# Kernel tuning notes

Measured on AMD Instinct MI355X. Metric: run time of the kernel, lower is better.

Reference implementation:

```python
import jax, jax.numpy as jnp
import numpy as np

N, L, D = 4, 4096, 1024
H = 16
HD = D // H          # 64
MLP = 4 * D          # 4096
EPS = 1e-5

def log_g(x):
    # torch: where(x>=0, log(relu(x)+0.5), -softplus(-x))
    return jnp.where(x >= 0.0, jnp.log(jax.nn.relu(x) + 0.5), -jax.nn.softplus(-x))

def parallel_scan_log(log_coeffs, log_values):
    # log_coeffs: (B, L, C); log_values: (B, L+1, C)
    a_star = jnp.pad(jnp.cumsum(log_coeffs, axis=1), ((0, 0), (1, 0), (0, 0)))
    log_h = jax.lax.cumlogsumexp(log_values - a_star, axis=1)
    return jnp.exp(a_star[:, 1:] + log_h[:, 1:])

def layer_norm(x, gamma, beta):
    mu = jnp.mean(x, axis=-1, keepdims=True)
    var = jnp.var(x, axis=-1, keepdims=True)
    return (x - mu) * jax.lax.rsqrt(var + EPS) * gamma + beta

def setup_inputs() -> dict:
    key = jax.random.key(0)
    ks = jax.random.split(key, 12)
    s = 0.02
    return {
        "x": jax.random.normal(ks[0], (N, L, D), jnp.float32),
        "h_0": jax.random.normal(ks[1], (N, 1, D), jnp.float32),
        "w_in": jax.random.normal(ks[2], (D, D), jnp.float32) * s,
        "b_in": jnp.zeros((D,), jnp.float32),
        "wz": jax.random.normal(ks[3], (HD, HD), jnp.float32) * s,
        "bz": jnp.zeros((HD,), jnp.float32),
        "wh": jax.random.normal(ks[4], (HD, HD), jnp.float32) * s,
        "bh": jnp.zeros((HD,), jnp.float32),
        "w_out": jax.random.normal(ks[5], (D, D), jnp.float32) * s,
        "b_out": jnp.zeros((D,), jnp.float32),
        "ln1_g": jnp.ones((D,), jnp.float32),
        "ln1_b": jnp.zeros((D,), jnp.float32),
        "ln2_g": jnp.ones((D,), jnp.float32),
        "ln2_b": jnp.zeros((D,), jnp.float32),
        "mw1": jax.random.normal(ks[6], (D, MLP), jnp.float32) * s,
        "mb1": jnp.zeros((MLP,), jnp.float32),
        "mw2": jax.random.normal(ks[7], (MLP, MLP), jnp.float32) * s,
        "mb2": jnp.zeros((MLP,), jnp.float32),
        "mw3": jax.random.normal(ks[8], (MLP, D), jnp.float32) * s,
        "mb3": jnp.zeros((D,), jnp.float32),
    }

def reference(x, h_0, w_in, b_in, wz, bz, wh, bh, w_out, b_out,
              ln1_g, ln1_b, ln2_g, ln2_b, mw1, mb1, mw2, mb2, mw3, mb3):
    n, l, d = x.shape
    rnn_input = layer_norm(x, ln1_g, ln1_b)
    pi = rnn_input @ w_in + b_in                                 # (N,L,D)
    pi = pi.reshape(n, l, H, HD).transpose(0, 2, 1, 3).reshape(n * H, l, HD)
    h0 = h_0.reshape(n, 1, H, HD).transpose(0, 2, 1, 3).reshape(n * H, 1, HD)
    # minGRU in log-space
    k = pi @ wz + bz
    log_z = -jax.nn.softplus(-k)
    log_coeffs = -jax.nn.softplus(k)
    log_h0 = log_g(h0)
    log_th = log_g(pi @ wh + bh)
    h = parallel_scan_log(log_coeffs, jnp.concatenate([log_h0, log_z + log_th], axis=1))
    rnn_states = h.reshape(n, H, l, HD).transpose(0, 2, 1, 3).reshape(n, l, d)
    x = x + (rnn_states @ w_out + b_out)
    mlp_in = layer_norm(x, ln2_g, ln2_b)
    y = jax.nn.silu(mlp_in @ mw1 + mb1)
    y = jax.nn.silu(y @ mw2 + mb2)
    y = y @ mw3 + mb3
    return (x + y, rnn_states)
```

## Files before the change

kernel.cpp:

```cpp
#include <hip/hip_runtime.h>
#include <hip/hip_bf16.h>

typedef __attribute__((ext_vector_type(8))) short short8;
typedef __attribute__((ext_vector_type(4))) float f32x4;
using bf16 = __hip_bfloat16;

#define DEV static __device__ __forceinline__

DEV float bf2f(bf16 v) { return __bfloat162float(v); }
DEV bf16 f2bf(float v) { return __float2bfloat16(v); }

DEV void gld_lds16(const void* g, void* l) {
  __builtin_amdgcn_global_load_lds(
      (const __attribute__((address_space(1))) void*)g,
      (__attribute__((address_space(3))) void*)l, 16, 0, 0);
}

__global__ __launch_bounds__(256)
void wconv_kernel(const float* __restrict__ w, bf16* __restrict__ wT, int K, int N) {
  __shared__ float tile[32][33];
  const int kt = blockIdx.x * 32, nt = blockIdx.y * 32;
  const int tx = threadIdx.x & 31, ty = threadIdx.x >> 5;
#pragma unroll
  for (int i = 0; i < 32; i += 8)
    tile[ty + i][tx] = w[(size_t)(kt + ty + i) * N + nt + tx];
  __syncthreads();
#pragma unroll
  for (int i = 0; i < 32; i += 8)
    wT[(size_t)(nt + ty + i) * K + kt + tx] = f2bf(tile[tx][ty + i]);
}

__global__ __launch_bounds__(256)
void ln_kernel(const float* __restrict__ x, const float* __restrict__ g,
               const float* __restrict__ b, bf16* __restrict__ out) {
  const int row = blockIdx.x;
  const int t = threadIdx.x;
  const float4 v = ((const float4*)(x + (size_t)row * 1024))[t];
  float s = v.x + v.y + v.z + v.w;
  float ss = v.x * v.x + v.y * v.y + v.z * v.z + v.w * v.w;
#pragma unroll
  for (int off = 32; off > 0; off >>= 1) {
    s += __shfl_down(s, off);
    ss += __shfl_down(ss, off);
  }
  __shared__ float red[8];
  if ((t & 63) == 0) { red[(t >> 6) * 2] = s; red[(t >> 6) * 2 + 1] = ss; }
  __syncthreads();
  s = red[0] + red[2] + red[4] + red[6];
  ss = red[1] + red[3] + red[5] + red[7];
  const float mu = s * (1.f / 1024.f);
  const float rstd = rsqrtf(ss * (1.f / 1024.f) - mu * mu + 1e-5f);
  const float4 g4 = ((const float4*)g)[t];
  const float4 b4 = ((const float4*)b)[t];
  struct alignas(8) B4 { bf16 v[4]; } o;
  o.v[0] = f2bf((v.x - mu) * rstd * g4.x + b4.x);
  o.v[1] = f2bf((v.y - mu) * rstd * g4.y + b4.y);
  o.v[2] = f2bf((v.z - mu) * rstd * g4.z + b4.z);
  o.v[3] = f2bf((v.w - mu) * rstd * g4.w + b4.w);
  *(B4*)(out + (size_t)row * 1024 + t * 4) = o;
}

template <int EPI>
__global__ __launch_bounds__(256, 2)
void gemm128(const bf16* __restrict__ A, const bf16* __restrict__ BT,
             const float* __restrict__ bias, const float* __restrict__ res,
             void* __restrict__ C, int M, int N, int K) {
  __shared__ short As[128 * 64];
  __shared__ short Bs[128 * 64];
  const int tid = threadIdx.x;
  const int l = tid & 63;
  const int w = tid >> 6;
  const int wr = w >> 1, wc = w & 1;

  const int nbn = N >> 7;
  const int nwg = gridDim.x;
  const int bid = blockIdx.x;
  const int q = nwg >> 3, r = nwg & 7;
  const int xcd = bid & 7, lin = bid >> 3;
  const int wg = (xcd < r ? xcd * (q + 1) : r * (q + 1) + (xcd - r) * q) + lin;
  const int bm = wg / nbn, bn = wg % nbn;

  const bf16* Ab = A + (size_t)bm * 128 * K;
  const bf16* Bb = BT + (size_t)bn * 128 * K;

  f32x4 acc[4][4];
#pragma unroll
  for (int i = 0; i < 4; ++i)
#pragma unroll
    for (int j = 0; j < 4; ++j) acc[i][j] = (f32x4){0.f, 0.f, 0.f, 0.f};

  const int srow = l >> 3;
  const int scol = (((l & 7) ^ (l >> 3)) << 3);

  for (int k0 = 0; k0 < K; k0 += 64) {
    __syncthreads();
#pragma unroll
    for (int p = 0; p < 4; ++p) {
      const int rowA = p * 32 + w * 8 + srow;
      gld_lds16(Ab + (size_t)rowA * K + k0 + scol, As + (p * 32 + w * 8) * 64);
      gld_lds16(Bb + (size_t)rowA * K + k0 + scol, Bs + (p * 32 + w * 8) * 64);
    }
    __syncthreads();
    const int xr = (l & 7) << 3;
#pragma unroll
    for (int kk = 0; kk < 2; ++kk) {
      short8 fa[4], fb[4];
#pragma unroll
      for (int m = 0; m < 4; ++m)
        fa[m] = *(const short8*)&As[(wr * 64 + m * 16 + (l & 15)) * 64 +
                                    ((kk * 32 + (l >> 4) * 8) ^ xr)];
#pragma unroll
      for (int n = 0; n < 4; ++n)
        fb[n] = *(const short8*)&Bs[(wc * 64 + n * 16 + (l & 15)) * 64 +
                                    ((kk * 32 + (l >> 4) * 8) ^ xr)];
#pragma unroll
      for (int m = 0; m < 4; ++m)
#pragma unroll
        for (int n = 0; n < 4; ++n)
          acc[m][n] = __builtin_amdgcn_mfma_f32_16x16x32_bf16(fa[m], fb[n], acc[m][n], 0, 0, 0);
    }
  }

  const int lc = l & 15;
  const int lr = (l >> 4) * 4;
#pragma unroll
  for (int n = 0; n < 4; ++n) {
    const int col = bn * 128 + wc * 64 + n * 16 + lc;
    const float bv = bias[col];
#pragma unroll
    for (int m = 0; m < 4; ++m) {
      const int row = bm * 128 + wr * 64 + m * 16 + lr;
#pragma unroll
      for (int r2 = 0; r2 < 4; ++r2) {
        float v = acc[m][n][r2] + bv;
        const size_t off = (size_t)(row + r2) * N + col;
        if constexpr (EPI == 1) v = v / (1.f + __expf(-v));
        if constexpr (EPI == 2) {
          ((float*)C)[off] = res[off] + v;
        } else {
          ((bf16*)C)[off] = f2bf(v);
        }
      }
    }
  }
  (void)M;
}

template <int EPI>
__global__ __launch_bounds__(512, 2)
void gemm256(const bf16* __restrict__ A, const bf16* __restrict__ BT,
             const float* __restrict__ bias, const float* __restrict__ res,
             void* __restrict__ C, int M, int N, int K) {
  __shared__ alignas(16) short As[2][256 * 64];
  __shared__ alignas(16) short Bs[2][256 * 64];
  const int tid = threadIdx.x;
  const int l = tid & 63;
  const int w = tid >> 6;
  const int wr = w >> 2;
  const int wc = w & 3;

  const int nbn = N >> 8;
  const int nwg = gridDim.x;
  const int bid = blockIdx.x;
  const int q = nwg >> 3, r = nwg & 7;
  const int xcd = bid & 7, lin = bid >> 3;
  const int wg = (xcd < r ? xcd * (q + 1) : r * (q + 1) + (xcd - r) * q) + lin;
  const int bm = wg / nbn, bn = wg % nbn;

  const bf16* Ab = A + (size_t)bm * 256 * K;
  const bf16* Bb = BT + (size_t)bn * 256 * K;

  const int gcol = ((l & 7) ^ (l >> 3)) << 3;
  const int fr = l & 15;
  const int kq = (l >> 4) << 3;
  const int xr = (l & 7) << 3;
  const int k0s = kq ^ xr;
  const int k1s = (32 + kq) ^ xr;

  const bf16* Abl = Ab + (size_t)(w * 16 + (l >> 3)) * K + gcol;
  const bf16* Bbl = Bb + (size_t)(w * 16 + (l >> 3)) * K + gcol;

  f32x4 acc[8][4];
#pragma unroll
  for (int i = 0; i < 8; ++i)
#pragma unroll
    for (int j = 0; j < 4; ++j) acc[i][j] = (f32x4){0.f, 0.f, 0.f, 0.f};

  short8 fa[2][2];
  short8 fb[4][2];

#define BARX() __builtin_amdgcn_s_barrier()
#define SBAR0() __builtin_amdgcn_sched_barrier(0)

#define STAGE_A(BUF, HALF, KT)                                                     \
  do {                                                                             \
    gld_lds16(Abl + (size_t)((HALF) * 128) * K + (size_t)(KT) * 64,                \
              &As[BUF][((HALF) * 128 + w * 16) * 64]);                             \
    gld_lds16(Abl + (size_t)((HALF) * 128 + 8) * K + (size_t)(KT) * 64,            \
              &As[BUF][((HALF) * 128 + w * 16 + 8) * 64]);                         \
  } while (0)

#define STAGE_B(BUF, HALF, KT)                                                     \
  do {                                                                             \
    gld_lds16(Bbl + (size_t)((HALF) * 128) * K + (size_t)(KT) * 64,                \
              &Bs[BUF][((HALF) * 128 + w * 16) * 64]);                             \
    gld_lds16(Bbl + (size_t)((HALF) * 128 + 8) * K + (size_t)(KT) * 64,            \
              &Bs[BUF][((HALF) * 128 + w * 16 + 8) * 64]);                         \
  } while (0)

#define RD_FA(BUF, Q)                                                                    \
  do {                                                                                  \
    fa[0][0] = *(const short8*)&As[BUF][(wr * 128 + (Q) * 32 + fr) * 64 + k0s];         \
    fa[0][1] = *(const short8*)&As[BUF][(wr * 128 + (Q) * 32 + fr) * 64 + k1s];         \
    fa[1][0] = *(const short8*)&As[BUF][(wr * 128 + (Q) * 32 + 16 + fr) * 64 + k0s];    \
    fa[1][1] = *(const short8*)&As[BUF][(wr * 128 + (Q) * 32 + 16 + fr) * 64 + k1s];    \
  } while (0)

#define RD_FB(BUF)                                                                      \
  do {                                                                                 \
    _Pragma("unroll") for (int n_ = 0; n_ < 4; ++n_) {                                 \
      fb[n_][0] = *(const short8*)&Bs[BUF][(wc * 64 + n_ * 16 + fr) * 64 + k0s];       \
      fb[n_][1] = *(const short8*)&Bs[BUF][(wc * 64 + n_ * 16 + fr) * 64 + k1s];       \
    }                                                                                  \
  } while (0)

#define MMA_Q(Q)                                                                        \
  do {                                                                                 \
    __builtin_amdgcn_s_setprio(1);                                                     \
    _Pragma("unroll") for (int n_ = 0; n_ < 4; ++n_) {                                 \
      acc[2 * (Q)][n_] = __builtin_amdgcn_mfma_f32_16x16x32_bf16(                      \
          fa[0][0], fb[n_][0], acc[2 * (Q)][n_], 0, 0, 0);                             \
      acc[2 * (Q) + 1][n_] = __builtin_amdgcn_mfma_f32_16x16x32_bf16(                  \
          fa[1][0], fb[n_][0], acc[2 * (Q) + 1][n_], 0, 0, 0);                         \
    }                                                                                  \
    _Pragma("unroll") for (int n_ = 0; n_ < 4; ++n_) {                                 \
      acc[2 * (Q)][n_] = __builtin_amdgcn_mfma_f32_16x16x32_bf16(                      \
          fa[0][1], fb[n_][1], acc[2 * (Q)][n_], 0, 0, 0);                             \
      acc[2 * (Q) + 1][n_] = __builtin_amdgcn_mfma_f32_16x16x32_bf16(                  \
          fa[1][1], fb[n_][1], acc[2 * (Q) + 1][n_], 0, 0, 0);                         \
    }                                                                                  \
    __builtin_amdgcn_s_setprio(0);                                                     \
  } while (0)

#define LGKM0() do { asm volatile("s_waitcnt lgkmcnt(0)"); SBAR0(); } while (0)

#define TILEBODY(BUF, T, HAVE_A, HAVE_B)                                               \
  do {                                                                                 \
                                                                     \
    RD_FB(BUF);                                                                        \
    RD_FA(BUF, 0);                                                                     \
    if (HAVE_A) STAGE_A((BUF) ^ 1, 0, (T) + 1);                                        \
    SBAR0();                                                                           \
    asm volatile("s_waitcnt lgkmcnt(8)");                                              \
    BARX();                                                                            \
    LGKM0();                                                                           \
    MMA_Q(0);                                                                          \
    BARX();                                                                            \
                                                                               \
    RD_FA(BUF, 1);                                                                     \
    if (HAVE_A) STAGE_A((BUF) ^ 1, 1, (T) + 1);                                        \
    SBAR0();                                                                           \
    BARX();                                                                            \
    LGKM0();                                                                           \
    MMA_Q(1);                                                                          \
    BARX();                                                                            \
                                                                               \
    RD_FA(BUF, 2);                                                                     \
    if (HAVE_B) STAGE_B(BUF, 0, (T) + 2);                                              \
    SBAR0();                                                                           \
    BARX();                                                                            \
    LGKM0();                                                                           \
    MMA_Q(2);                                                                          \
    BARX();                                                                            \
                                                                               \
    RD_FA(BUF, 3);                                                                     \
    if (HAVE_B) STAGE_B(BUF, 1, (T) + 2);                                              \
    SBAR0();                                                                           \
    BARX();                                                                            \
    LGKM0();                                                                           \
    MMA_Q(3);                                                                          \
    if (HAVE_B) asm volatile("s_waitcnt vmcnt(4)" ::: "memory");                       \
    else        asm volatile("s_waitcnt vmcnt(0)" ::: "memory");                       \
    BARX();                                                                            \
  } while (0)

  STAGE_A(0, 0, 0); STAGE_A(0, 1, 0);
  STAGE_B(0, 0, 0); STAGE_B(0, 1, 0);
  STAGE_B(1, 0, 1); STAGE_B(1, 1, 1);
  asm volatile("s_waitcnt vmcnt(4)" ::: "memory");
  BARX();

  const int NT = K >> 6;
  const int NI = NT >> 1;
#pragma unroll 1
  for (int i = 0; i < NI; ++i) {
    const int t0 = 2 * i;
    const bool mb0 = (t0 + 2) < NT;
    const bool mb1 = (t0 + 3) < NT;
    TILEBODY(0, t0, true, mb0);
    TILEBODY(1, t0 + 1, mb0, mb1);
  }

#undef BARX
#undef SBAR0
#undef STAGE_A
#undef STAGE_B
#undef RD_FA
#undef RD_FB
#undef MMA_Q
#undef LGKM0
#undef TILEBODY

  const int lc = l & 15;
  const int lr = (l >> 4) * 4;
#pragma unroll
  for (int n = 0; n < 4; ++n) {
    const int col = bn * 256 + wc * 64 + n * 16 + lc;
    const float bv = bias[col];
#pragma unroll
    for (int m = 0; m < 8; ++m) {
      const int row = bm * 256 + wr * 128 + m * 16 + lr;
#pragma unroll
      for (int r2 = 0; r2 < 4; ++r2) {
        float v = acc[m][n][r2] + bv;
        const size_t off = (size_t)(row + r2) * N + col;
        if constexpr (EPI == 1) v = v / (1.f + __expf(-v));
        if constexpr (EPI == 2) {
          ((float*)C)[off] = res[off] + v;
        } else {
          ((bf16*)C)[off] = f2bf(v);
        }
      }
    }
  }
  (void)M;
}

__global__ __launch_bounds__(256)
void heads_kernel(const bf16* __restrict__ piB,
                  const float* __restrict__ wz, const float* __restrict__ bz,
                  const float* __restrict__ wh, const float* __restrict__ bh,
                  bf16* __restrict__ aB, bf16* __restrict__ bB) {
  __shared__ float wzs[4096], whs[4096], pis[4096];
  const int h = blockIdx.y;
  const int t0 = blockIdx.x * 64;
  const int tid = threadIdx.x;
#pragma unroll
  for (int i = tid; i < 4096; i += 256) {
    wzs[i] = wz[i];
    whs[i] = wh[i];
    pis[i] = bf2f(piB[(size_t)(t0 + (i >> 6)) * 1024 + h * 64 + (i & 63)]);
  }
  __syncthreads();
  const int hd = tid & 63;
  const int tb = (tid >> 6) * 16;
  float accK[16], accT[16];
  const float bzv = bz[hd], bhv = bh[hd];
#pragma unroll
  for (int i = 0; i < 16; ++i) { accK[i] = bzv; accT[i] = bhv; }
  for (int j = 0; j < 64; ++j) {
    const float wzv = wzs[j * 64 + hd];
    const float whv = whs[j * 64 + hd];
#pragma unroll
    for (int i = 0; i < 16; ++i) {
      const float p = pis[(tb + i) * 64 + j];
      accK[i] = fmaf(p, wzv, accK[i]);
      accT[i] = fmaf(p, whv, accT[i]);
    }
  }
#pragma unroll
  for (int i = 0; i < 16; ++i) {
    const float k = accK[i], th = accT[i];
    const float sig = 1.f / (1.f + __expf(-k));
    const float a = 1.f - sig;
    const float gg = th >= 0.f ? th + 0.5f : 1.f / (1.f + __expf(-th));
    const float bb = sig * gg;
    const size_t idx = (size_t)(t0 + tb + i) * 1024 + h * 64 + hd;
    aB[idx] = f2bf(a);
    bB[idx] = f2bf(bb);
  }
}

__global__ __launch_bounds__(256)
void scan_phase1(const bf16* __restrict__ aB, const bf16* __restrict__ bB,
                 float* __restrict__ cA, float* __restrict__ cB) {
  const int idx = blockIdx.x * 256 + threadIdx.x;
  const int c = idx & 1023;
  const int chunk = (idx >> 10) & 63;
  const int n = idx >> 16;
  size_t base = ((size_t)(n * 4096 + chunk * 64)) * 1024 + c;
  float A = 1.f, B = 0.f;
#pragma unroll 8
  for (int s = 0; s < 64; ++s) {
    const float a = bf2f(aB[base]);
    const float b = bf2f(bB[base]);
    A *= a;
    B = fmaf(a, B, b);
    base += 1024;
  }
  const size_t o = ((size_t)(n * 64 + chunk)) * 1024 + c;
  cA[o] = A;
  cB[o] = B;
}

__global__ __launch_bounds__(256)
void scan_phase2(const float* __restrict__ h0,
                 const float* __restrict__ cA, const float* __restrict__ cB,
                 float* __restrict__ hst) {
  const int idx = blockIdx.x * 256 + threadIdx.x;
  const int c = idx & 1023;
  const int n = idx >> 10;
  float hv = h0[(size_t)n * 1024 + c];
  hv = hv >= 0.f ? hv + 0.5f : 1.f / (1.f + __expf(-hv));
  for (int ch = 0; ch < 64; ++ch) {
    const size_t o = ((size_t)(n * 64 + ch)) * 1024 + c;
    hst[o] = hv;
    hv = fmaf(cA[o], hv, cB[o]);
  }
}

__global__ __launch_bounds__(256)
void scan_phase3(const bf16* __restrict__ aB, const bf16* __restrict__ bB,
                 const float* __restrict__ hst,
                 float* __restrict__ rnn, bf16* __restrict__ rnnB) {
  const int idx = blockIdx.x * 256 + threadIdx.x;
  const int c = idx & 1023;
  const int chunk = (idx >> 10) & 63;
  const int n = idx >> 16;
  float hv = hst[((size_t)(n * 64 + chunk)) * 1024 + c];
  size_t base = ((size_t)(n * 4096 + chunk * 64)) * 1024 + c;
#pragma unroll 4
  for (int s = 0; s < 64; ++s) {
    const float a = bf2f(aB[base]);
    const float b = bf2f(bB[base]);
    hv = fmaf(a, hv, b);
    rnn[base] = hv;
    rnnB[base] = f2bf(hv);
    base += 1024;
  }
}

extern "C" void kernel_launch(void* const* d_in, const int* in_sizes, int n_in,
                              void* d_out, int out_size, void* d_ws, size_t ws_size,
                              hipStream_t stream) {
  const float* x    = (const float*)d_in[0];
  const float* h0   = (const float*)d_in[1];
  const float* w_in = (const float*)d_in[2];
  const float* b_in = (const float*)d_in[3];
  const float* wz   = (const float*)d_in[4];
  const float* bz   = (const float*)d_in[5];
  const float* wh   = (const float*)d_in[6];
  const float* bh   = (const float*)d_in[7];
  const float* w_out= (const float*)d_in[8];
  const float* b_out= (const float*)d_in[9];
  const float* ln1g = (const float*)d_in[10];
  const float* ln1b = (const float*)d_in[11];
  const float* ln2g = (const float*)d_in[12];
  const float* ln2b = (const float*)d_in[13];
  const float* mw1  = (const float*)d_in[14];
  const float* mb1  = (const float*)d_in[15];
  const float* mw2  = (const float*)d_in[16];
  const float* mb2  = (const float*)d_in[17];
  const float* mw3  = (const float*)d_in[18];
  const float* mb3  = (const float*)d_in[19];
  (void)in_sizes; (void)n_in; (void)out_size;

  float* out0 = (float*)d_out;
  float* out1 = (float*)d_out + (size_t)16384 * 1024;

  char* ws = (char*)d_ws;
  size_t o = 0;
  auto take = [&](size_t bytes) { char* p = ws + o; o += (bytes + 255) & ~(size_t)255; return p; };
  bf16* w_inT = (bf16*)take((size_t)1024 * 1024 * 2);
  bf16* w_outT= (bf16*)take((size_t)1024 * 1024 * 2);
  bf16* mw1T  = (bf16*)take((size_t)4096 * 1024 * 2);
  bf16* mw2T  = (bf16*)take((size_t)4096 * 4096 * 2);
  bf16* mw3T  = (bf16*)take((size_t)4096 * 1024 * 2);
  bf16* lnxB  = (bf16*)take((size_t)16384 * 1024 * 2);
  bf16* piB   = (bf16*)take((size_t)16384 * 1024 * 2);
  bf16* aB    = (bf16*)take((size_t)16384 * 1024 * 2);
  bf16* bB    = (bf16*)take((size_t)16384 * 1024 * 2);
  float* cA   = (float*)take((size_t)4 * 64 * 1024 * 4);
  float* cB   = (float*)take((size_t)4 * 64 * 1024 * 4);
  float* hst  = (float*)take((size_t)4 * 64 * 1024 * 4);
  if (o > ws_size) return;

  wconv_kernel<<<dim3(32, 32), 256, 0, stream>>>(w_in, w_inT, 1024, 1024);
  wconv_kernel<<<dim3(32, 32), 256, 0, stream>>>(w_out, w_outT, 1024, 1024);
  wconv_kernel<<<dim3(32, 128), 256, 0, stream>>>(mw1, mw1T, 1024, 4096);
  wconv_kernel<<<dim3(128, 128), 256, 0, stream>>>(mw2, mw2T, 4096, 4096);
  wconv_kernel<<<dim3(128, 32), 256, 0, stream>>>(mw3, mw3T, 4096, 1024);

  ln_kernel<<<16384, 256, 0, stream>>>(x, ln1g, ln1b, lnxB);
  gemm256<0><<<256, 512, 0, stream>>>(lnxB, w_inT, b_in, nullptr, piB, 16384, 1024, 1024);

  heads_kernel<<<dim3(256, 16), 256, 0, stream>>>(piB, wz, bz, wh, bh, aB, bB);
  scan_phase1<<<1024, 256, 0, stream>>>(aB, bB, cA, cB);
  scan_phase2<<<16, 256, 0, stream>>>(h0, cA, cB, hst);
  scan_phase3<<<1024, 256, 0, stream>>>(aB, bB, hst, out1, lnxB );

  gemm256<2><<<256, 512, 0, stream>>>(lnxB, w_outT, b_out, x, out0, 16384, 1024, 1024);

  ln_kernel<<<16384, 256, 0, stream>>>(out0, ln2g, ln2b, lnxB );
  bf16* t1 = aB;
  bf16* t2 = bB;
  for (int mc = 0; mc < 4; ++mc) {
    const bf16* a3 = lnxB + (size_t)mc * 4096 * 1024;
    gemm256<1><<<256, 512, 0, stream>>>(a3, mw1T, mb1, nullptr, t1, 4096, 4096, 1024);
    gemm256<1><<<256, 512, 0, stream>>>(t1, mw2T, mb2, nullptr, t2, 4096, 4096, 4096);
    float* oc = out0 + (size_t)mc * 4096 * 1024;
    gemm128<2><<<256, 256, 0, stream>>>(t2, mw3T, mb3, oc, oc, 4096, 1024, 4096);
  }
}
```

Before: 1.356 ms.

## Reschedule GEMM main loop to prefetch next tile fragments during MMA

Reorders the per-tile GEMM pipeline so each quarter of MFMA work is issued first, followed by the LDS fragment reads for the next quarter. It also pulls the next buffer's B and A0 fragment reads into the tail of the current tile. Both A-stage loads are issued after the first MMA quarter, and the separate lgkmcnt(8) wait and several barriers are dropped. The intent is to hide LDS read latency and cut barrier count. In exchange, vmcnt accounting gets tighter and the buffer-hazard ordering becomes riskier.

```diff
diff --git a/kernel.cpp b/kernel.cpp
--- a/kernel.cpp
+++ b/kernel.cpp
@@ -244,44 +244,38 @@
 
 #define LGKM0() do { asm volatile("s_waitcnt lgkmcnt(0)"); SBAR0(); } while (0)
 
-#define TILEBODY(BUF, T, HAVE_A, HAVE_B)                                               \
+#define TILE(BUF, T, HASA, HASB)                                                       \
   do {                                                                                 \
-                                                                     \
-    RD_FB(BUF);                                                                        \
-    RD_FA(BUF, 0);                                                                     \
-    if (HAVE_A) STAGE_A((BUF) ^ 1, 0, (T) + 1);                                        \
-    SBAR0();                                                                           \
-    asm volatile("s_waitcnt lgkmcnt(8)");                                              \
-    BARX();                                                                            \
+                                                                               \
     LGKM0();                                                                           \
     MMA_Q(0);                                                                          \
-    BARX();                                                                            \
+    if (HASA) { STAGE_A((BUF) ^ 1, 0, (T) + 1); STAGE_A((BUF) ^ 1, 1, (T) + 1); }      \
+    RD_FA(BUF, 1);                                                                     \
+    SBAR0(); BARX();                                                                   \
                                                                                \
-    RD_FA(BUF, 1);                                                                     \
-    if (HAVE_A) STAGE_A((BUF) ^ 1, 1, (T) + 1);                                        \
-    SBAR0();                                                                           \
-    BARX();                                                                            \
     LGKM0();                                                                           \
     MMA_Q(1);                                                                          \
-    BARX();                                                                            \
+    RD_FA(BUF, 2);                                                                     \
+    SBAR0(); BARX();                                                                   \
                                                                                \
-    RD_FA(BUF, 2);                                                                     \
-    if (HAVE_B) STAGE_B(BUF, 0, (T) + 2);                                              \
-    SBAR0();                                                                           \
-    BARX();                                                                            \
     LGKM0();                                                                           \
     MMA_Q(2);                                                                          \
-    BARX();                                                                            \
+    if (HASB) STAGE_B(BUF, 0, (T) + 2);                                                \
+    if (HASA) {                                                                        \
+      if (HASB) asm volatile("s_waitcnt vmcnt(2)" ::: "memory");                       \
+      else      asm volatile("s_waitcnt vmcnt(0)" ::: "memory");                       \
+    }                                                                                  \
+    RD_FA(BUF, 3);                                                                     \
+    SBAR0(); BARX();                                                                   \
                                                                                \
-    RD_FA(BUF, 3);                                                                     \
-    if (HAVE_B) STAGE_B(BUF, 1, (T) + 2);                                              \
-    SBAR0();                                                                           \
-    BARX();                                                                            \
     LGKM0();                                                                           \
     MMA_Q(3);                                                                          \
-    if (HAVE_B) asm volatile("s_waitcnt vmcnt(4)" ::: "memory");                       \
-    else        asm volatile("s_waitcnt vmcnt(0)" ::: "memory");                       \
-    BARX();                                                                            \
+    if (HASB) STAGE_B(BUF, 1, (T) + 2);                                                \
+    if (HASA) {                                                                        \
+      RD_FB((BUF) ^ 1);                                                                \
+      RD_FA((BUF) ^ 1, 0);                                                             \
+      SBAR0(); BARX();                                                                 \
+    }                                                                                  \
   } while (0)
 
   STAGE_A(0, 0, 0); STAGE_A(0, 1, 0);
@@ -289,16 +283,18 @@
   STAGE_B(1, 0, 1); STAGE_B(1, 1, 1);
   asm volatile("s_waitcnt vmcnt(4)" ::: "memory");
   BARX();
+  RD_FB(0);
+  RD_FA(0, 0);
 
   const int NT = K >> 6;
   const int NI = NT >> 1;
 #pragma unroll 1
   for (int i = 0; i < NI; ++i) {
     const int t0 = 2 * i;
-    const bool mb0 = (t0 + 2) < NT;
-    const bool mb1 = (t0 + 3) < NT;
-    TILEBODY(0, t0, true, mb0);
-    TILEBODY(1, t0 + 1, mb0, mb1);
+    const bool b0 = (t0 + 2) < NT;
+    const bool b1 = (t0 + 3) < NT;
+    TILE(0, t0, true, b0);
+    TILE(1, t0 + 1, b0, b1);
   }
 
 #undef BARX
@@ -309,7 +305,7 @@
 #undef RD_FB
 #undef MMA_Q
 #undef LGKM0
-#undef TILEBODY
+#undef TILE
 
   const int lc = l & 15;
   const int lr = (l >> 4) * 4;
```

After: 1.376 ms. About the same (+1.5%).
